# Kernel tuning notes

Measured on AMD Instinct MI355X. Metric: run time of the kernel, lower is better.

Reference implementation:

```python
import jax, jax.numpy as jnp
import numpy as np

B, S, D = 2, 2048, 2048
H, KVH, HD = 16, 4, 128
GROUPS = H // KVH
SCALE = HD ** -0.5


def rotate_half(x):
    half = x.shape[-1] // 2
    return jnp.concatenate((-x[..., half:], x[..., :half]), axis=-1)


def apply_rope(q, k, cos, sin):
    # q,k: [B,S,H,HD]; cos,sin: [S,HD//2] -> repeat_interleave(2) -> [S,HD]
    cos = jnp.repeat(cos, 2, axis=-1)[None, :, None, :]
    sin = jnp.repeat(sin, 2, axis=-1)[None, :, None, :]
    return q * cos + rotate_half(q) * sin, k * cos + rotate_half(k) * sin


def setup_inputs() -> dict:
    key = jax.random.key(0)
    ks = jax.random.split(key, 8)
    inp = {
        'x': jax.random.normal(ks[0], (B, S, D), dtype=jnp.float32),
        'cos': jnp.cos(jnp.arange(S, dtype=jnp.float32)[:, None] * (1.0 / (10000.0 ** (jnp.arange(HD // 2, dtype=jnp.float32) / (HD // 2))))[None, :].reshape(1, HD // 2)),
        'sin': None,
        'mask': jnp.tril(jnp.ones((S, S), dtype=bool))[None, None, :, :],
        'Wq': jax.random.normal(ks[1], (D, H * HD), dtype=jnp.float32) * (D ** -0.5),
        'Wk': jax.random.normal(ks[2], (D, KVH * HD), dtype=jnp.float32) * (D ** -0.5),
        'Wv': jax.random.normal(ks[3], (D, KVH * HD), dtype=jnp.float32) * (D ** -0.5),
        'Wo': jax.random.normal(ks[4], (H * HD, D), dtype=jnp.float32) * ((H * HD) ** -0.5),
    }
    inv_freq = 1.0 / (10000.0 ** (jnp.arange(0, HD // 2, dtype=jnp.float32) / (HD // 2)))
    freqs = jnp.arange(S, dtype=jnp.float32)[:, None] * inv_freq[None, :]  # [S, HD//2]
    inp['cos'] = jnp.cos(freqs)
    inp['sin'] = jnp.sin(freqs)
    return inp


def reference(x, cos, sin, mask, Wq, Wk, Wv, Wo):
    b, s, _ = x.shape
    q = (x @ Wq).reshape(b, s, H, HD)    # [B,S,H,HD]
    k = (x @ Wk).reshape(b, s, KVH, HD)  # [B,S,KVH,HD]
    v = (x @ Wv).reshape(b, s, KVH, HD)
    q, k = apply_rope(q, k, cos, sin)
    q = q.transpose(0, 2, 1, 3)  # [B,H,S,HD]
    k = k.transpose(0, 2, 1, 3)  # [B,KVH,S,HD]
    v = v.transpose(0, 2, 1, 3)
    k = jnp.repeat(k, GROUPS, axis=1)  # [B,H,S,HD]
    v = jnp.repeat(v, GROUPS, axis=1)
    scores = jnp.einsum('bhqd,bhkd->bhqk', q, k) * SCALE
    scores = jnp.where(mask, scores, -jnp.inf)
    attn = jax.nn.softmax(scores, axis=-1)
    out = jnp.einsum('bhqk,bhkd->bhqd', attn, v)
    out = out.transpose(0, 2, 1, 3).reshape(b, s, H * HD)
    return out @ Wo
```

## Files before the change

kernel.cpp:

```cpp
#include <hip/hip_runtime.h>
#include <hip/hip_bf16.h>
#include <cstdint>
#include <type_traits>

typedef __attribute__((ext_vector_type(8))) short short8;
typedef __attribute__((ext_vector_type(4))) float floatx4;

constexpr int S_LEN = 2048;
constexpr float ATTN_SCALE = 0.08838834764831845f;
constexpr float LOG2E = 1.4426950408889634f;
constexpr float CP = ATTN_SCALE * LOG2E;
constexpr float THRR = 5.0f / CP;

__device__ __forceinline__ void gl_lds16(const void* gp, void* lp) {
  __builtin_amdgcn_global_load_lds(
      (__attribute__((address_space(1))) void*)(uintptr_t)gp,
      (__attribute__((address_space(3))) void*)lp,
      16, 0, 0);
}

__device__ __forceinline__ void rope8(short8 x0, short8 x1, const float* ca,
                                      const float* sa, const float* cb,
                                      const float* sb, short8& y0, short8& y1) {
#pragma unroll
  for (int e = 0; e < 8; ++e) {
    union { short s; __hip_bfloat16 h; } u0, u1, w0, w1;
    u0.s = x0[e]; u1.s = x1[e];
    float f0 = __bfloat162float(u0.h), f1 = __bfloat162float(u1.h);
    int j = e >> 1;
    w0.h = __float2bfloat16(f0 * ca[j] - f1 * sa[j]);
    w1.h = __float2bfloat16(f1 * cb[j] + f0 * sb[j]);
    y0[e] = w0.s; y1[e] = w1.s;
  }
}

__device__ __forceinline__ void tr32(const float* __restrict__ src,
                                     __hip_bfloat16* __restrict__ dst,
                                     int blk, int nblk_x, int N, int tid,
                                     float (*tile)[33]) {
  int n0 = (blk % nblk_x) * 32, k0 = (blk / nblk_x) * 32;
  int tx = tid & 31, ty = tid >> 5;
#pragma unroll
  for (int i = ty; i < 32; i += 8)
    tile[i][tx] = src[(size_t)(k0 + i) * N + n0 + tx];
  __syncthreads();
#pragma unroll
  for (int i = ty; i < 32; i += 8)
    dst[(size_t)(n0 + i) * 2048 + k0 + tx] = __float2bfloat16(tile[tx][i]);
}

__global__ void prep_kernel(const float* __restrict__ x,
                            const float* __restrict__ Wq,
                            const float* __restrict__ Wk,
                            const float* __restrict__ Wv,
                            const float* __restrict__ Wo,
                            __hip_bfloat16* __restrict__ xb,
                            __hip_bfloat16* __restrict__ wqkvt,
                            __hip_bfloat16* __restrict__ wot) {
  __shared__ float tile[32][33];
  int bx = blockIdx.x, tid = threadIdx.x;
  if (bx < 8192) {
    int i = bx * 256 + tid;
    float4 f = reinterpret_cast<const float4*>(x)[i];
    union { unsigned long long u64; __hip_bfloat16 h[4]; } u;
    u.h[0] = __float2bfloat16(f.x);
    u.h[1] = __float2bfloat16(f.y);
    u.h[2] = __float2bfloat16(f.z);
    u.h[3] = __float2bfloat16(f.w);
    reinterpret_cast<unsigned long long*>(xb)[i] = u.u64;
  } else if (bx < 12288) {
    tr32(Wq, wqkvt, bx - 8192, 64, 2048, tid, tile);
  } else if (bx < 13312) {
    tr32(Wk, wqkvt + 2048 * 2048, bx - 12288, 16, 512, tid, tile);
  } else if (bx < 14336) {
    tr32(Wv, wqkvt + 2560 * 2048, bx - 13312, 16, 512, tid, tile);
  } else {
    tr32(Wo, wot, bx - 14336, 64, 2048, tid, tile);
  }
}

__device__ __forceinline__ void gemm256_core(
    const __hip_bfloat16* __restrict__ Ab,
    const __hip_bfloat16* __restrict__ Bb,
    const int K, __hip_bfloat16* lds, floatx4 (&acc)[8][4]) {
  const int tid = threadIdx.x;
  const int wave = tid >> 6, lane = tid & 63;
  const int quad = lane >> 4, l15 = lane & 15;
  const int wm = wave >> 2, wn = wave & 3;
  const int nt = K >> 6;
  const int u2 = wave * 2;

  auto stA = [&](int tt, int h) {
    __hip_bfloat16* dst = lds + (tt & 1) * 32768;
    const int k0 = tt << 6;
#pragma unroll
    for (int j = 0; j < 2; ++j) {
      const int kc = (u2 + j) >> 1, rb = (u2 + j) & 1;
      gl_lds16(Ab + (size_t)(h * 128 + rb * 64 + lane) * K + k0 + kc * 8,
               dst + (kc * 256 + h * 128 + rb * 64) * 8);
    }
  };
  auto stB = [&](int tt, int h) {
    __hip_bfloat16* dst = lds + (tt & 1) * 32768 + 16384;
    const int k0 = tt << 6;
#pragma unroll
    for (int j = 0; j < 2; ++j) {
      const int kc = (u2 + j) >> 1, rb = (u2 + j) & 1;
      gl_lds16(Bb + (size_t)(h * 128 + rb * 64 + lane) * K + k0 + kc * 8,
               dst + (kc * 256 + h * 128 + rb * 64) * 8);
    }
  };

  stA(0, 0); stA(0, 1); stB(0, 0); stB(0, 1);
  if (nt > 1) { stB(1, 0); stB(1, 1); }
  asm volatile("s_waitcnt vmcnt(4)" ::: "memory");
  __builtin_amdgcn_s_barrier();

  const int abase = (quad * 256 + wm * 128 + l15) * 8;
  const int bbase = (quad * 256 + wn * 64 + l15) * 8;

#pragma unroll 2
  for (int t = 0; t < nt; ++t) {
    const __hip_bfloat16* Al = lds + (t & 1) * 32768;
    const __hip_bfloat16* Bl = Al + 16384;
    short8 b[2][4];
#pragma unroll
    for (int q = 0; q < 4; ++q) {
      short8 a[2][2];
#pragma unroll
      for (int kk = 0; kk < 2; ++kk) {
        if (q == 0) {
#pragma unroll
          for (int ni = 0; ni < 4; ++ni)
            b[kk][ni] = *(const short8*)&Bl[kk * 8192 + bbase + ni * 128];
        }
#pragma unroll
        for (int mi = 0; mi < 2; ++mi)
          a[kk][mi] = *(const short8*)&Al[kk * 8192 + abase + (2 * q + mi) * 128];
      }
      if (q == 0)      { if (t + 1 < nt) stA(t + 1, 0); }
      else if (q == 1) { if (t + 1 < nt) stA(t + 1, 1); }
      else if (q == 2) { if (t + 2 < nt) stB(t + 2, 0); }
      else             { if (t + 2 < nt) stB(t + 2, 1); }
      __builtin_amdgcn_s_barrier();
      asm volatile("s_waitcnt lgkmcnt(0)" ::: "memory");
      __builtin_amdgcn_sched_barrier(0);
      __builtin_amdgcn_s_setprio(1);
#pragma unroll
      for (int kk = 0; kk < 2; ++kk)
#pragma unroll
        for (int mi = 0; mi < 2; ++mi)
#pragma unroll
          for (int ni = 0; ni < 4; ++ni)
            acc[2 * q + mi][ni] = __builtin_amdgcn_mfma_f32_16x16x32_bf16(
                a[kk][mi], b[kk][ni], acc[2 * q + mi][ni], 0, 0, 0);
      __builtin_amdgcn_s_setprio(0);
      if (q == 3) {
        if (t + 2 < nt) asm volatile("s_waitcnt vmcnt(4)" ::: "memory");
        else            asm volatile("s_waitcnt vmcnt(0)" ::: "memory");
      }
      __builtin_amdgcn_s_barrier();
    }
  }
  asm volatile("" ::: "memory");
}

__device__ __forceinline__ void gemm_256x128_core(
    const __hip_bfloat16* __restrict__ Ab,
    const __hip_bfloat16* __restrict__ Bb,
    const int K, __hip_bfloat16* lds, floatx4 (&acc)[4][4]) {
  const int tid = threadIdx.x;
  const int wave = tid >> 6, lane = tid & 63;
  const int quad = lane >> 4, l15 = lane & 15;
  const int wm = wave >> 1, wn = wave & 1;
  const int nt = K >> 6;

  auto stA = [&](int tt, int c) {
    __hip_bfloat16* dst = lds + (tt & 1) * 24576;
    const int k0 = tt << 6;
    const int i = c * 8 + wave;
    const int kc = i >> 2, rb = i & 3;
    gl_lds16(Ab + (size_t)(rb * 64 + lane) * K + k0 + kc * 8,
             dst + (kc * 256 + rb * 64) * 8);
  };
  auto stB = [&](int tt, int c) {
    __hip_bfloat16* dst = lds + (tt & 1) * 24576 + 16384;
    const int k0 = tt << 6;
    const int i = c * 8 + wave;
    const int kc = i >> 1, rb = i & 1;
    gl_lds16(Bb + (size_t)(rb * 64 + lane) * K + k0 + kc * 8,
             dst + (kc * 128 + rb * 64) * 8);
  };

  stA(0, 0); stA(0, 1); stA(0, 2); stA(0, 3);
  stB(0, 0); stB(0, 1);
  if (nt > 1) {
    stB(1, 0); stB(1, 1);
    asm volatile("s_waitcnt vmcnt(2)" ::: "memory");
  } else {
    asm volatile("s_waitcnt vmcnt(0)" ::: "memory");
  }
  __builtin_amdgcn_s_barrier();

  const int abase = (quad * 256 + wm * 64 + l15) * 8;
  const int bbase = (quad * 128 + wn * 64 + l15) * 8;

#pragma unroll 2
  for (int t = 0; t < nt; ++t) {
    const __hip_bfloat16* Al = lds + (t & 1) * 24576;
    const __hip_bfloat16* Bl = Al + 16384;
    short8 b[2][4], a[2][2];
#pragma unroll
    for (int kk = 0; kk < 2; ++kk) {
#pragma unroll
      for (int ni = 0; ni < 4; ++ni)
        b[kk][ni] = *(const short8*)&Bl[kk * 4096 + bbase + ni * 128];
#pragma unroll
      for (int mi = 0; mi < 2; ++mi)
        a[kk][mi] = *(const short8*)&Al[kk * 8192 + abase + mi * 128];
    }
    if (t + 1 < nt) { stA(t + 1, 0); stA(t + 1, 1); }
    __builtin_amdgcn_s_barrier();
    asm volatile("s_waitcnt lgkmcnt(0)" ::: "memory");
    __builtin_amdgcn_sched_barrier(0);
    __builtin_amdgcn_s_setprio(1);
#pragma unroll
    for (int kk = 0; kk < 2; ++kk)
#pragma unroll
      for (int mi = 0; mi < 2; ++mi)
#pragma unroll
        for (int ni = 0; ni < 4; ++ni)
          acc[mi][ni] = __builtin_amdgcn_mfma_f32_16x16x32_bf16(
              a[kk][mi], b[kk][ni], acc[mi][ni], 0, 0, 0);
    __builtin_amdgcn_s_setprio(0);
    __builtin_amdgcn_s_barrier();
#pragma unroll
    for (int kk = 0; kk < 2; ++kk)
#pragma unroll
      for (int mi = 0; mi < 2; ++mi)
        a[kk][mi] = *(const short8*)&Al[kk * 8192 + abase + (2 + mi) * 128];
    if (t + 1 < nt) { stA(t + 1, 2); stA(t + 1, 3); }
    if (t + 2 < nt) { stB(t + 2, 0); stB(t + 2, 1); }
    __builtin_amdgcn_s_barrier();
    asm volatile("s_waitcnt lgkmcnt(0)" ::: "memory");
    __builtin_amdgcn_sched_barrier(0);
    __builtin_amdgcn_s_setprio(1);
#pragma unroll
    for (int kk = 0; kk < 2; ++kk)
#pragma unroll
      for (int mi = 0; mi < 2; ++mi)
#pragma unroll
        for (int ni = 0; ni < 4; ++ni)
          acc[2 + mi][ni] = __builtin_amdgcn_mfma_f32_16x16x32_bf16(
              a[kk][mi], b[kk][ni], acc[2 + mi][ni], 0, 0, 0);
    __builtin_amdgcn_s_setprio(0);
    if (t + 2 < nt) asm volatile("s_waitcnt vmcnt(2)" ::: "memory");
    else            asm volatile("s_waitcnt vmcnt(0)" ::: "memory");
    __builtin_amdgcn_s_barrier();
  }
  asm volatile("" ::: "memory");
}

__global__ __launch_bounds__(512, 2) void qkv_gemm_kernel(
    const __hip_bfloat16* __restrict__ A,
    const __hip_bfloat16* __restrict__ Bt,
    __hip_bfloat16* __restrict__ qbuf,
    __hip_bfloat16* __restrict__ kbuf,
    __hip_bfloat16* __restrict__ vbuf,
    const float* __restrict__ cosb,
    const float* __restrict__ sinb) {
  constexpr int K = 2048;
  __shared__ __align__(16) __hip_bfloat16 lds[65536];
  const int tid = threadIdx.x;
  const int m0 = blockIdx.y * 256, n0 = blockIdx.x * 256;

  floatx4 acc[8][4] = {};
  gemm256_core(A + (size_t)m0 * K, Bt + (size_t)n0 * K, K, lds, acc);

  const int wave = tid >> 6, lane = tid & 63;
  const int quad = lane >> 4, l15 = lane & 15;
  const int wm = wave >> 2, wn = wave & 3;
  const bool isv = (n0 >= 2560);
  short* lds2 = (short*)lds;
#pragma unroll
  for (int mi = 0; mi < 8; ++mi)
#pragma unroll
    for (int ni = 0; ni < 4; ++ni)
#pragma unroll
      for (int r = 0; r < 4; ++r) {
        int row = wm * 128 + mi * 16 + quad * 4 + r;
        int col = wn * 64 + ni * 16 + l15;
        union { short s; __hip_bfloat16 h; } u;
        u.h = __float2bfloat16(acc[mi][ni][r]);
        if (isv) lds2[col * 256 + row] = u.s;
        else     lds2[row * 256 + col] = u.s;
      }
  __syncthreads();

  const int c16 = tid & 15, hh = c16 >> 3, c8 = c16 & 7;
  const int rid = tid >> 4, d0 = c8 * 8;
  if (n0 < 2048) {
#pragma unroll
    for (int j = 0; j < 8; ++j) {
      int rr = rid + 32 * j;
      int rowg = m0 + rr;
      int s = rowg & (S_LEN - 1);
      float ca[4], sa[4], cb[4], sb[4];
      *(float4*)ca = *(const float4*)&cosb[s * 64 + c8 * 4];
      *(float4*)sa = *(const float4*)&sinb[s * 64 + c8 * 4];
      *(float4*)cb = *(const float4*)&cosb[s * 64 + 32 + c8 * 4];
      *(float4*)sb = *(const float4*)&sinb[s * 64 + 32 + c8 * 4];
      short8 x0 = *(const short8*)&lds2[rr * 256 + hh * 128 + d0];
      short8 x1 = *(const short8*)&lds2[rr * 256 + hh * 128 + 64 + d0];
      short8 y0, y1;
      rope8(x0, x1, ca, sa, cb, sb, y0, y1);
      *(short8*)(qbuf + (size_t)rowg * 2048 + n0 + hh * 128 + d0) = y0;
      *(short8*)(qbuf + (size_t)rowg * 2048 + n0 + hh * 128 + 64 + d0) = y1;
    }
  } else if (!isv) {
    const int kvh = ((n0 - 2048) >> 7) + hh;
#pragma unroll
    for (int j = 0; j < 8; ++j) {
      int rr = rid + 32 * j;
      int rowg = m0 + rr;
      int s = rowg & (S_LEN - 1), bb = rowg >> 11;
      int kv = s & 63;
      size_t tb = ((size_t)(bb * 4 + kvh) * 32 + (s >> 6)) * 8192;
      float ca[4], sa[4], cb[4], sb[4];
      *(float4*)ca = *(const float4*)&cosb[s * 64 + c8 * 4];
      *(float4*)sa = *(const float4*)&sinb[s * 64 + c8 * 4];
      *(float4*)cb = *(const float4*)&cosb[s * 64 + 32 + c8 * 4];
      *(float4*)sb = *(const float4*)&sinb[s * 64 + 32 + c8 * 4];
      short8 x0 = *(const short8*)&lds2[rr * 256 + hh * 128 + d0];
      short8 x1 = *(const short8*)&lds2[rr * 256 + hh * 128 + 64 + d0];
      short8 y0, y1;
      rope8(x0, x1, ca, sa, cb, sb, y0, y1);
      *(short8*)(kbuf + tb + (size_t)c8 * 512 + kv * 8) = y0;
      *(short8*)(kbuf + tb + (size_t)(8 + c8) * 512 + kv * 8) = y1;
    }
  } else {
    const int kvh = ((n0 - 2560) >> 7) + hh;
    const int bb = m0 >> 11;
    const int kt0 = (m0 & (S_LEN - 1)) >> 6;
    const int kv0 = c8 * 8;
#pragma unroll
    for (int j = 0; j < 4; ++j) {
      int d = rid + 32 * j;
      int cxor = (d & 7) << 3;
#pragma unroll
      for (int half = 0; half < 4; ++half) {
        short8 vv = *(const short8*)&lds2[(hh * 128 + d) * 256 + half * 64 + kv0];
        size_t tb = ((size_t)(bb * 4 + kvh) * 32 + kt0 + half) * 8192;
        *(short8*)(vbuf + tb + d * 64 + (kv0 ^ cxor)) = vv;
      }
    }
  }
}

__global__ __launch_bounds__(512, 2) void gemm_bt_f32_kernel(
    const __hip_bfloat16* __restrict__ A,
    const __hip_bfloat16* __restrict__ Bt,
    float* __restrict__ C, int N, int K) {
  __shared__ __align__(16) __hip_bfloat16 lds[49152];
  const int tid = threadIdx.x;
  const int m0 = blockIdx.y * 256, n0 = blockIdx.x * 128;

  floatx4 acc[4][4] = {};
  gemm_256x128_core(A + (size_t)m0 * K, Bt + (size_t)n0 * K, K, lds, acc);

  const int wave = tid >> 6, lane = tid & 63;
  const int quad = lane >> 4, l15 = lane & 15;
  const int wm = wave >> 1, wn = wave & 1;
#pragma unroll
  for (int mi = 0; mi < 4; ++mi)
#pragma unroll
    for (int ni = 0; ni < 4; ++ni)
#pragma unroll
      for (int r = 0; r < 4; ++r) {
        int row = m0 + wm * 64 + mi * 16 + quad * 4 + r;
        int col = n0 + wn * 64 + ni * 16 + l15;
        C[(size_t)row * N + col] = acc[mi][ni][r];
      }
}

__global__ __launch_bounds__(256, 2) void attn_kernel(
    const __hip_bfloat16* __restrict__ qbuf,
    const __hip_bfloat16* __restrict__ kbuf,
    const __hip_bfloat16* __restrict__ vbuf,
    __hip_bfloat16* __restrict__ aout) {
  const int qt = (blockIdx.y & 16) ? blockIdx.x : (15 - blockIdx.x);
  const int bh = blockIdx.y;
  const int b = bh >> 4, h = bh & 15;
  const int kvh = h >> 2;

  __shared__ __align__(16) __hip_bfloat16 Kbuf[2][8192];
  __shared__ __align__(16) __hip_bfloat16 Vbuf[2][8192];

  const int tid = threadIdx.x;
  const int wave = tid >> 6, lane = tid & 63;
  const int quad = lane >> 4, l15 = lane & 15;

  short8 qfrag[2][4];
#pragma unroll
  for (int rs = 0; rs < 2; ++rs)
#pragma unroll
    for (int kc = 0; kc < 4; ++kc)
      qfrag[rs][kc] = *(const short8*)(qbuf +
          (size_t)(b * S_LEN + qt * 128 + rs * 64 + wave * 16 + l15) * 2048 +
          h * 128 + kc * 32 + quad * 8);

  const __hip_bfloat16* ktiles = kbuf + (size_t)(b * 4 + kvh) * 32 * 8192;
  const __hip_bfloat16* vtiles = vbuf + (size_t)(b * 4 + kvh) * 32 * 8192;
  const int nt = 2 * qt + 2;

#pragma unroll
  for (int j = 0; j < 4; ++j) {
    int c = tid + 256 * j;
    gl_lds16(ktiles + c * 8, &Kbuf[0][c * 8]);
    gl_lds16(vtiles + c * 8, &Vbuf[0][c * 8]);
  }

  float m_s[2] = {-1e30f, -1e30f};
  float l_s[2] = {0.f, 0.f};
  floatx4 o[2][8] = {};

  for (int kt = 0; kt < nt; ++kt) {
    const int cur = kt & 1;
    __syncthreads();

    if (kt + 1 < nt) {
      const __hip_bfloat16* kb = ktiles + (size_t)(kt + 1) * 8192;
      const __hip_bfloat16* vb = vtiles + (size_t)(kt + 1) * 8192;
#pragma unroll
      for (int j = 0; j < 4; ++j) {
        int c = tid + 256 * j;
        gl_lds16(kb + c * 8, &Kbuf[1 - cur][c * 8]);
        gl_lds16(vb + c * 8, &Vbuf[1 - cur][c * 8]);
      }
    }

    floatx4 sc[2][4] = {};
#pragma unroll
    for (int ni = 0; ni < 4; ++ni)
#pragma unroll
      for (int kc = 0; kc < 4; ++kc) {
        short8 bf = *(const short8*)&Kbuf[cur][((kc * 4 + quad) * 64 + ni * 16 + l15) * 8];
        sc[0][ni] = __builtin_amdgcn_mfma_f32_16x16x32_bf16(bf, qfrag[0][kc], sc[0][ni], 0, 0, 0);
        sc[1][ni] = __builtin_amdgcn_mfma_f32_16x16x32_bf16(bf, qfrag[1][kc], sc[1][ni], 0, 0, 0);
      }

    short8 pa[2][2];
#pragma unroll
    for (int rs = 0; rs < 2; ++rs) {
      const int qt64 = 2 * qt + rs;
      if (kt >= qt64) {
        const int qg = qt * 128 + rs * 64 + wave * 16 + l15;
#pragma unroll
        for (int ni = 0; ni < 4; ++ni) {
          int kvb = kt * 64 + ni * 16 + quad * 4;
#pragma unroll
          for (int r = 0; r < 4; ++r)
            if (kvb + r > qg) sc[rs][ni][r] = -1e30f;
        }
      }

      float v = sc[rs][0][0];
#pragma unroll
      for (int ni = 0; ni < 4; ++ni)
#pragma unroll
        for (int r = 0; r < 4; ++r) v = fmaxf(v, sc[rs][ni][r]);
      v = fmaxf(v, __shfl_xor(v, 16));
      v = fmaxf(v, __shfl_xor(v, 32));

      float mold = m_s[rs];
      if (__any(v > mold + THRR)) {
        float mnew = fmaxf(mold, v);
        float alpha = exp2f((mold - mnew) * CP);
        m_s[rs] = mnew;
        l_s[rs] *= alpha;
        float ar[4];
#pragma unroll
        for (int r = 0; r < 4; ++r)
          ar[r] = __shfl(alpha, (lane & 48) + quad * 4 + r);
#pragma unroll
        for (int nc = 0; nc < 8; ++nc)
#pragma unroll
          for (int r = 0; r < 4; ++r) o[rs][nc][r] *= ar[r];
      }

      float mc = m_s[rs] * CP;
      unsigned pk[4][2];
      float lsum = 0.f;
#pragma unroll
      for (int ni = 0; ni < 4; ++ni)
#pragma unroll
        for (int pr = 0; pr < 2; ++pr) {
          float p0 = exp2f(sc[rs][ni][2 * pr] * CP - mc);
          float p1 = exp2f(sc[rs][ni][2 * pr + 1] * CP - mc);
          lsum += p0 + p1;
          union { unsigned u; ushort us[2]; } uu;
          union { __hip_bfloat16 h; ushort us; } b0, b1;
          b0.h = __float2bfloat16(p0); b1.h = __float2bfloat16(p1);
          uu.us[0] = b0.us; uu.us[1] = b1.us;
          pk[ni][pr] = uu.u;
        }
      lsum += __shfl_xor(lsum, 16);
      lsum += __shfl_xor(lsum, 32);
      l_s[rs] += lsum;

#pragma unroll
      for (int kk2 = 0; kk2 < 2; ++kk2) {
        union { unsigned w[4]; short8 s; } pw_;
#pragma unroll
        for (int j = 0; j < 4; ++j) {
          int src = ((((quad & 1) * 2) + (j >> 1)) << 4) | l15;
          unsigned lo = (unsigned)__shfl((int)pk[2 * kk2][j & 1], src);
          unsigned hi = (unsigned)__shfl((int)pk[2 * kk2 + 1][j & 1], src);
          pw_.w[j] = (quad >> 1) ? hi : lo;
        }
        pa[rs][kk2] = pw_.s;
      }
    }

#pragma unroll
    for (int kk2 = 0; kk2 < 2; ++kk2) {
#pragma unroll
      for (int nc = 0; nc < 8; ++nc) {
        int d = nc * 16 + l15;
        int swcol = (kk2 * 32 + quad * 8) ^ ((d & 7) << 3);
        short8 vv = *(const short8*)&Vbuf[cur][d * 64 + swcol];
        o[0][nc] = __builtin_amdgcn_mfma_f32_16x16x32_bf16(pa[0][kk2], vv, o[0][nc], 0, 0, 0);
        o[1][nc] = __builtin_amdgcn_mfma_f32_16x16x32_bf16(pa[1][kk2], vv, o[1][nc], 0, 0, 0);
      }
    }
  }

#pragma unroll
  for (int rs = 0; rs < 2; ++rs) {
    float inv[4];
#pragma unroll
    for (int r = 0; r < 4; ++r) {
      float lr = __shfl(l_s[rs], (lane & 48) + quad * 4 + r);
      inv[r] = 1.0f / lr;
    }
    const size_t orow0 = (size_t)(b * S_LEN + qt * 128 + rs * 64 + wave * 16 + quad * 4);
#pragma unroll
    for (int nc = 0; nc < 8; ++nc)
#pragma unroll
      for (int r = 0; r < 4; ++r)
        aout[(orow0 + r) * 2048 + h * 128 + nc * 16 + l15] =
            __float2bfloat16(o[rs][nc][r] * inv[r]);
  }
}

extern "C" void kernel_launch(void* const* d_in, const int* in_sizes, int n_in,
                              void* d_out, int out_size, void* d_ws, size_t ws_size,
                              hipStream_t stream) {
  const float* x    = (const float*)d_in[0];
  const float* cosb = (const float*)d_in[1];
  const float* sinb = (const float*)d_in[2];
  const float* Wq = (const float*)d_in[4];
  const float* Wk = (const float*)d_in[5];
  const float* Wv = (const float*)d_in[6];
  const float* Wo = (const float*)d_in[7];
  float* out = (float*)d_out;

  char* ws = (char*)d_ws;
  __hip_bfloat16* xb    = (__hip_bfloat16*)(ws);
  __hip_bfloat16* wqkvt = (__hip_bfloat16*)(ws + (16u << 20));
  __hip_bfloat16* wot   = (__hip_bfloat16*)(ws + (28u << 20));
  __hip_bfloat16* qbuf  = (__hip_bfloat16*)(ws + (36u << 20));
  __hip_bfloat16* kbuf  = (__hip_bfloat16*)(ws + (52u << 20));
  __hip_bfloat16* vbuf  = (__hip_bfloat16*)(ws + (56u << 20));
  __hip_bfloat16* aout  = (__hip_bfloat16*)(ws + (60u << 20));

  prep_kernel<<<18432, 256, 0, stream>>>(x, Wq, Wk, Wv, Wo, xb, wqkvt, wot);
  qkv_gemm_kernel<<<dim3(12, 16), 512, 0, stream>>>(xb, wqkvt, qbuf, kbuf, vbuf, cosb, sinb);
  attn_kernel<<<dim3(16, 32), 256, 0, stream>>>(qbuf, kbuf, vbuf, aout);
  gemm_bt_f32_kernel<<<dim3(16, 16), 512, 0, stream>>>(aout, wot, out, 2048, 2048);
}
```

Measured before the change: 366.7 us.

## Software-pipeline QK of next tile with softmax/PV, split K/V prefetch barriers

Restructures the attention inner loop so the QK^T MFMAs for tile i+1 are issued before softmax and PV of tile i, letting matrix work overlap the softmax math. K and V loads are issued separately with explicit vmcnt waits and raw barriers, so each buffer is refilled as soon as it is free. It also skips MFMAs for the first 64-row half once that half is fully masked, and raises wave priority around the PV MFMAs. This adds register pressure from the extra score accumulators and relies on hand-counted vmcnt values being correct.

```diff
diff --git a/kernel.cpp b/kernel.cpp
--- a/kernel.cpp
+++ b/kernel.cpp
@@ -413,51 +413,65 @@
   const __hip_bfloat16* vtiles = vbuf + (size_t)(b * 4 + kvh) * 32 * 8192;
   const int nt = 2 * qt + 2;
 
-#pragma unroll
-  for (int j = 0; j < 4; ++j) {
-    int c = tid + 256 * j;
-    gl_lds16(ktiles + c * 8, &Kbuf[0][c * 8]);
-    gl_lds16(vtiles + c * 8, &Vbuf[0][c * 8]);
-  }
+  auto SK = [&](int t) {
+#pragma unroll
+    for (int j = 0; j < 4; ++j) {
+      int c = tid + 256 * j;
+      gl_lds16(ktiles + (size_t)t * 8192 + c * 8, &Kbuf[t & 1][c * 8]);
+    }
+  };
+  auto SV = [&](int t) {
+#pragma unroll
+    for (int j = 0; j < 4; ++j) {
+      int c = tid + 256 * j;
+      gl_lds16(vtiles + (size_t)t * 8192 + c * 8, &Vbuf[t & 1][c * 8]);
+    }
+  };
+
+  auto QK = [&](const __hip_bfloat16* Kc, floatx4 (&s)[2][4], bool q0) {
+#pragma unroll
+    for (int ni = 0; ni < 4; ++ni)
+#pragma unroll
+      for (int kc = 0; kc < 4; ++kc) {
+        short8 bf = *(const short8*)&Kc[((kc * 4 + quad) * 64 + ni * 16 + l15) * 8];
+        if (q0)
+          s[0][ni] = __builtin_amdgcn_mfma_f32_16x16x32_bf16(bf, qfrag[0][kc], s[0][ni], 0, 0, 0);
+        s[1][ni] = __builtin_amdgcn_mfma_f32_16x16x32_bf16(bf, qfrag[1][kc], s[1][ni], 0, 0, 0);
+      }
+  };
+
+  SK(0); SV(0);
+  SK(1); SV(1);
+  asm volatile("s_waitcnt vmcnt(12)" ::: "memory");
+  __builtin_amdgcn_s_barrier();
 
   float m_s[2] = {-1e30f, -1e30f};
   float l_s[2] = {0.f, 0.f};
   floatx4 o[2][8] = {};
 
-  for (int kt = 0; kt < nt; ++kt) {
-    const int cur = kt & 1;
-    __syncthreads();
-
-    if (kt + 1 < nt) {
-      const __hip_bfloat16* kb = ktiles + (size_t)(kt + 1) * 8192;
-      const __hip_bfloat16* vb = vtiles + (size_t)(kt + 1) * 8192;
-#pragma unroll
-      for (int j = 0; j < 4; ++j) {
-        int c = tid + 256 * j;
-        gl_lds16(kb + c * 8, &Kbuf[1 - cur][c * 8]);
-        gl_lds16(vb + c * 8, &Vbuf[1 - cur][c * 8]);
-      }
-    }
-
-    floatx4 sc[2][4] = {};
-#pragma unroll
-    for (int ni = 0; ni < 4; ++ni)
-#pragma unroll
-      for (int kc = 0; kc < 4; ++kc) {
-        short8 bf = *(const short8*)&Kbuf[cur][((kc * 4 + quad) * 64 + ni * 16 + l15) * 8];
-        sc[0][ni] = __builtin_amdgcn_mfma_f32_16x16x32_bf16(bf, qfrag[0][kc], sc[0][ni], 0, 0, 0);
-        sc[1][ni] = __builtin_amdgcn_mfma_f32_16x16x32_bf16(bf, qfrag[1][kc], sc[1][ni], 0, 0, 0);
-      }
-
+  floatx4 sc[2][4] = {};
+  QK(Kbuf[0], sc, true);
+
+  for (int i = 0; i < nt; ++i) {
+    if (i + 1 < nt) asm volatile("s_waitcnt vmcnt(4)" ::: "memory");
+    else            asm volatile("s_waitcnt vmcnt(0)" ::: "memory");
+    __builtin_amdgcn_s_barrier();
+    if (i + 2 < nt) SK(i + 2);
+
+    floatx4 sc2[2][4] = {};
+    if (i + 1 < nt) QK(Kbuf[(i + 1) & 1], sc2, (i + 1) <= 2 * qt);
+
+    const bool do0 = (i <= 2 * qt);
     short8 pa[2][2];
 #pragma unroll
     for (int rs = 0; rs < 2; ++rs) {
+      if (rs == 0 && !do0) continue;
       const int qt64 = 2 * qt + rs;
-      if (kt >= qt64) {
+      if (i >= qt64) {
         const int qg = qt * 128 + rs * 64 + wave * 16 + l15;
 #pragma unroll
         for (int ni = 0; ni < 4; ++ni) {
-          int kvb = kt * 64 + ni * 16 + quad * 4;
+          int kvb = i * 64 + ni * 16 + quad * 4;
 #pragma unroll
           for (int r = 0; r < 4; ++r)
             if (kvb + r > qg) sc[rs][ni][r] = -1e30f;
@@ -522,17 +536,29 @@
       }
     }
 
+    __builtin_amdgcn_s_setprio(1);
 #pragma unroll
     for (int kk2 = 0; kk2 < 2; ++kk2) {
 #pragma unroll
       for (int nc = 0; nc < 8; ++nc) {
         int d = nc * 16 + l15;
         int swcol = (kk2 * 32 + quad * 8) ^ ((d & 7) << 3);
-        short8 vv = *(const short8*)&Vbuf[cur][d * 64 + swcol];
-        o[0][nc] = __builtin_amdgcn_mfma_f32_16x16x32_bf16(pa[0][kk2], vv, o[0][nc], 0, 0, 0);
+        short8 vv = *(const short8*)&Vbuf[i & 1][d * 64 + swcol];
+        if (do0)
+          o[0][nc] = __builtin_amdgcn_mfma_f32_16x16x32_bf16(pa[0][kk2], vv, o[0][nc], 0, 0, 0);
         o[1][nc] = __builtin_amdgcn_mfma_f32_16x16x32_bf16(pa[1][kk2], vv, o[1][nc], 0, 0, 0);
       }
     }
+    __builtin_amdgcn_s_setprio(0);
+
+    asm volatile("" ::: "memory");
+    __builtin_amdgcn_s_barrier();
+    if (i + 2 < nt) SV(i + 2);
+
+#pragma unroll
+    for (int rs = 0; rs < 2; ++rs)
+#pragma unroll
+      for (int ni = 0; ni < 4; ++ni) sc[rs][ni] = sc2[rs][ni];
   }
 
 #pragma unroll
```

Measured after the change: 383.0 us. +4.5%, slower.

## Halve attention query tile, read V fragments directly from global memory

Applied to the files above, without the earlier changes.

The attention kernel now processes 64 query rows per block instead of 128, doubling the grid and raising the occupancy hint to 4 blocks per CU. V is no longer staged through LDS. The QKV epilogue writes V in an MFMA-fragment-ready layout so each lane loads its B operand straight from global memory, with raised wave priority around the PV MFMAs. This trades LDS usage and sync cost for more parallelism, but reloads K/V tiles twice as often across blocks and puts global-load latency directly in the PV loop.

```diff
diff --git a/kernel.cpp b/kernel.cpp
--- a/kernel.cpp
+++ b/kernel.cpp
@@ -346,12 +346,12 @@
 #pragma unroll
     for (int j = 0; j < 4; ++j) {
       int d = rid + 32 * j;
-      int cxor = (d & 7) << 3;
 #pragma unroll
       for (int half = 0; half < 4; ++half) {
         short8 vv = *(const short8*)&lds2[(hh * 128 + d) * 256 + half * 64 + kv0];
         size_t tb = ((size_t)(bb * 4 + kvh) * 32 + kt0 + half) * 8192;
-        *(short8*)(vbuf + tb + d * 64 + (kv0 ^ cxor)) = vv;
+        *(short8*)(vbuf + tb + ((c8 >> 2) * 8 + (d >> 4)) * 512
+                        + ((c8 & 3) * 16 + (d & 15)) * 8) = vv;
       }
     }
   }
@@ -383,174 +383,153 @@
       }
 }
 
-__global__ __launch_bounds__(256, 2) void attn_kernel(
+__global__ __launch_bounds__(256, 4) void attn_kernel(
     const __hip_bfloat16* __restrict__ qbuf,
     const __hip_bfloat16* __restrict__ kbuf,
     const __hip_bfloat16* __restrict__ vbuf,
     __hip_bfloat16* __restrict__ aout) {
-  const int qt = (blockIdx.y & 16) ? blockIdx.x : (15 - blockIdx.x);
+  const int qt = (blockIdx.y & 16) ? blockIdx.x : (31 - blockIdx.x);
   const int bh = blockIdx.y;
   const int b = bh >> 4, h = bh & 15;
   const int kvh = h >> 2;
 
   __shared__ __align__(16) __hip_bfloat16 Kbuf[2][8192];
-  __shared__ __align__(16) __hip_bfloat16 Vbuf[2][8192];
 
   const int tid = threadIdx.x;
   const int wave = tid >> 6, lane = tid & 63;
   const int quad = lane >> 4, l15 = lane & 15;
 
-  short8 qfrag[2][4];
-#pragma unroll
-  for (int rs = 0; rs < 2; ++rs)
-#pragma unroll
-    for (int kc = 0; kc < 4; ++kc)
-      qfrag[rs][kc] = *(const short8*)(qbuf +
-          (size_t)(b * S_LEN + qt * 128 + rs * 64 + wave * 16 + l15) * 2048 +
-          h * 128 + kc * 32 + quad * 8);
+  short8 qfrag[4];
+#pragma unroll
+  for (int kc = 0; kc < 4; ++kc)
+    qfrag[kc] = *(const short8*)(qbuf +
+        (size_t)(b * S_LEN + qt * 64 + wave * 16 + l15) * 2048 +
+        h * 128 + kc * 32 + quad * 8);
 
   const __hip_bfloat16* ktiles = kbuf + (size_t)(b * 4 + kvh) * 32 * 8192;
   const __hip_bfloat16* vtiles = vbuf + (size_t)(b * 4 + kvh) * 32 * 8192;
-  const int nt = 2 * qt + 2;
-
-#pragma unroll
-  for (int j = 0; j < 4; ++j) {
-    int c = tid + 256 * j;
-    gl_lds16(ktiles + c * 8, &Kbuf[0][c * 8]);
-    gl_lds16(vtiles + c * 8, &Vbuf[0][c * 8]);
-  }
-
-  float m_s[2] = {-1e30f, -1e30f};
-  float l_s[2] = {0.f, 0.f};
-  floatx4 o[2][8] = {};
-
-  for (int kt = 0; kt < nt; ++kt) {
-    const int cur = kt & 1;
+  const int nt = qt + 1;
+
+  auto SK = [&](int t) {
+#pragma unroll
+    for (int j = 0; j < 4; ++j) {
+      int c = tid + 256 * j;
+      gl_lds16(ktiles + (size_t)t * 8192 + c * 8, &Kbuf[t & 1][c * 8]);
+    }
+  };
+
+  SK(0);
+
+  float m_s = -1e30f, l_s = 0.f;
+  floatx4 o[8] = {};
+
+  for (int i = 0; i < nt; ++i) {
     __syncthreads();
-
-    if (kt + 1 < nt) {
-      const __hip_bfloat16* kb = ktiles + (size_t)(kt + 1) * 8192;
-      const __hip_bfloat16* vb = vtiles + (size_t)(kt + 1) * 8192;
+    if (i + 1 < nt) SK(i + 1);
+
+    floatx4 sc[4] = {};
+#pragma unroll
+    for (int ni = 0; ni < 4; ++ni)
+#pragma unroll
+      for (int kc = 0; kc < 4; ++kc) {
+        short8 bf = *(const short8*)&Kbuf[i & 1][((kc * 4 + quad) * 64 + ni * 16 + l15) * 8];
+        sc[ni] = __builtin_amdgcn_mfma_f32_16x16x32_bf16(bf, qfrag[kc], sc[ni], 0, 0, 0);
+      }
+
+    if (i == qt) {
+      const int qg = qt * 64 + wave * 16 + l15;
+#pragma unroll
+      for (int ni = 0; ni < 4; ++ni) {
+        int kvb = i * 64 + ni * 16 + quad * 4;
+#pragma unroll
+        for (int r = 0; r < 4; ++r)
+          if (kvb + r > qg) sc[ni][r] = -1e30f;
+      }
+    }
+
+    float v = sc[0][0];
+#pragma unroll
+    for (int ni = 0; ni < 4; ++ni)
+#pragma unroll
+      for (int r = 0; r < 4; ++r) v = fmaxf(v, sc[ni][r]);
+    v = fmaxf(v, __shfl_xor(v, 16));
+    v = fmaxf(v, __shfl_xor(v, 32));
+
+    float mold = m_s;
+    if (__any(v > mold + THRR)) {
+      float mnew = fmaxf(mold, v);
+      float alpha = exp2f((mold - mnew) * CP);
+      m_s = mnew;
+      l_s *= alpha;
+      float ar[4];
+#pragma unroll
+      for (int r = 0; r < 4; ++r)
+        ar[r] = __shfl(alpha, (lane & 48) + quad * 4 + r);
+#pragma unroll
+      for (int nc = 0; nc < 8; ++nc)
+#pragma unroll
+        for (int r = 0; r < 4; ++r) o[nc][r] *= ar[r];
+    }
+
+    float mc = m_s * CP;
+    unsigned pk[4][2];
+    float lsum = 0.f;
+#pragma unroll
+    for (int ni = 0; ni < 4; ++ni)
+#pragma unroll
+      for (int pr = 0; pr < 2; ++pr) {
+        float p0 = exp2f(sc[ni][2 * pr] * CP - mc);
+        float p1 = exp2f(sc[ni][2 * pr + 1] * CP - mc);
+        lsum += p0 + p1;
+        union { unsigned u; ushort us[2]; } uu;
+        union { __hip_bfloat16 h; ushort us; } b0, b1;
+        b0.h = __float2bfloat16(p0); b1.h = __float2bfloat16(p1);
+        uu.us[0] = b0.us; uu.us[1] = b1.us;
+        pk[ni][pr] = uu.u;
+      }
+    lsum += __shfl_xor(lsum, 16);
+    lsum += __shfl_xor(lsum, 32);
+    l_s += lsum;
+
+    short8 pa[2];
+#pragma unroll
+    for (int kk2 = 0; kk2 < 2; ++kk2) {
+      union { unsigned w[4]; short8 s; } pw_;
 #pragma unroll
       for (int j = 0; j < 4; ++j) {
-        int c = tid + 256 * j;
-        gl_lds16(kb + c * 8, &Kbuf[1 - cur][c * 8]);
-        gl_lds16(vb + c * 8, &Vbuf[1 - cur][c * 8]);
-      }
-    }
-
-    floatx4 sc[2][4] = {};
-#pragma unroll
-    for (int ni = 0; ni < 4; ++ni)
-#pragma unroll
-      for (int kc = 0; kc < 4; ++kc) {
-        short8 bf = *(const short8*)&Kbuf[cur][((kc * 4 + quad) * 64 + ni * 16 + l15) * 8];
-        sc[0][ni] = __builtin_amdgcn_mfma_f32_16x16x32_bf16(bf, qfrag[0][kc], sc[0][ni], 0, 0, 0);
-        sc[1][ni] = __builtin_amdgcn_mfma_f32_16x16x32_bf16(bf, qfrag[1][kc], sc[1][ni], 0, 0, 0);
-      }
-
-    short8 pa[2][2];
-#pragma unroll
-    for (int rs = 0; rs < 2; ++rs) {
-      const int qt64 = 2 * qt + rs;
-      if (kt >= qt64) {
-        const int qg = qt * 128 + rs * 64 + wave * 16 + l15;
-#pragma unroll
-        for (int ni = 0; ni < 4; ++ni) {
-          int kvb = kt * 64 + ni * 16 + quad * 4;
-#pragma unroll
-          for (int r = 0; r < 4; ++r)
-            if (kvb + r > qg) sc[rs][ni][r] = -1e30f;
-        }
-      }
-
-      float v = sc[rs][0][0];
-#pragma unroll
-      for (int ni = 0; ni < 4; ++ni)
-#pragma unroll
-        for (int r = 0; r < 4; ++r) v = fmaxf(v, sc[rs][ni][r]);
-      v = fmaxf(v, __shfl_xor(v, 16));
-      v = fmaxf(v, __shfl_xor(v, 32));
-
-      float mold = m_s[rs];
-      if (__any(v > mold + THRR)) {
-        float mnew = fmaxf(mold, v);
-        float alpha = exp2f((mold - mnew) * CP);
-        m_s[rs] = mnew;
-        l_s[rs] *= alpha;
-        float ar[4];
-#pragma unroll
-        for (int r = 0; r < 4; ++r)
-          ar[r] = __shfl(alpha, (lane & 48) + quad * 4 + r);
-#pragma unroll
-        for (int nc = 0; nc < 8; ++nc)
-#pragma unroll
-          for (int r = 0; r < 4; ++r) o[rs][nc][r] *= ar[r];
-      }
-
-      float mc = m_s[rs] * CP;
-      unsigned pk[4][2];
-      float lsum = 0.f;
-#pragma unroll
-      for (int ni = 0; ni < 4; ++ni)
-#pragma unroll
-        for (int pr = 0; pr < 2; ++pr) {
-          float p0 = exp2f(sc[rs][ni][2 * pr] * CP - mc);
-          float p1 = exp2f(sc[rs][ni][2 * pr + 1] * CP - mc);
-          lsum += p0 + p1;
-          union { unsigned u; ushort us[2]; } uu;
-          union { __hip_bfloat16 h; ushort us; } b0, b1;
-          b0.h = __float2bfloat16(p0); b1.h = __float2bfloat16(p1);
-          uu.us[0] = b0.us; uu.us[1] = b1.us;
-          pk[ni][pr] = uu.u;
-        }
-      lsum += __shfl_xor(lsum, 16);
-      lsum += __shfl_xor(lsum, 32);
-      l_s[rs] += lsum;
-
-#pragma unroll
-      for (int kk2 = 0; kk2 < 2; ++kk2) {
-        union { unsigned w[4]; short8 s; } pw_;
-#pragma unroll
-        for (int j = 0; j < 4; ++j) {
-          int src = ((((quad & 1) * 2) + (j >> 1)) << 4) | l15;
-          unsigned lo = (unsigned)__shfl((int)pk[2 * kk2][j & 1], src);
-          unsigned hi = (unsigned)__shfl((int)pk[2 * kk2 + 1][j & 1], src);
-          pw_.w[j] = (quad >> 1) ? hi : lo;
-        }
-        pa[rs][kk2] = pw_.s;
-      }
-    }
-
-#pragma unroll
-    for (int kk2 = 0; kk2 < 2; ++kk2) {
+        int src = ((((quad & 1) * 2) + (j >> 1)) << 4) | l15;
+        unsigned lo = (unsigned)__shfl((int)pk[2 * kk2][j & 1], src);
+        unsigned hi = (unsigned)__shfl((int)pk[2 * kk2 + 1][j & 1], src);
+        pw_.w[j] = (quad >> 1) ? hi : lo;
+      }
+      pa[kk2] = pw_.s;
+    }
+
+    const __hip_bfloat16* vt = vtiles + (size_t)i * 8192;
+    __builtin_amdgcn_s_setprio(1);
+#pragma unroll
+    for (int kk2 = 0; kk2 < 2; ++kk2)
 #pragma unroll
       for (int nc = 0; nc < 8; ++nc) {
-        int d = nc * 16 + l15;
-        int swcol = (kk2 * 32 + quad * 8) ^ ((d & 7) << 3);
-        short8 vv = *(const short8*)&Vbuf[cur][d * 64 + swcol];
-        o[0][nc] = __builtin_amdgcn_mfma_f32_16x16x32_bf16(pa[0][kk2], vv, o[0][nc], 0, 0, 0);
-        o[1][nc] = __builtin_amdgcn_mfma_f32_16x16x32_bf16(pa[1][kk2], vv, o[1][nc], 0, 0, 0);
-      }
-    }
-  }
-
-#pragma unroll
-  for (int rs = 0; rs < 2; ++rs) {
-    float inv[4];
-#pragma unroll
-    for (int r = 0; r < 4; ++r) {
-      float lr = __shfl(l_s[rs], (lane & 48) + quad * 4 + r);
-      inv[r] = 1.0f / lr;
-    }
-    const size_t orow0 = (size_t)(b * S_LEN + qt * 128 + rs * 64 + wave * 16 + quad * 4);
-#pragma unroll
-    for (int nc = 0; nc < 8; ++nc)
-#pragma unroll
-      for (int r = 0; r < 4; ++r)
-        aout[(orow0 + r) * 2048 + h * 128 + nc * 16 + l15] =
-            __float2bfloat16(o[rs][nc][r] * inv[r]);
-  }
+        short8 vv = *(const short8*)&vt[((kk2 * 8 + nc) * 64 + quad * 16 + l15) * 8];
+        o[nc] = __builtin_amdgcn_mfma_f32_16x16x32_bf16(pa[kk2], vv, o[nc], 0, 0, 0);
+      }
+    __builtin_amdgcn_s_setprio(0);
+  }
+
+  float inv[4];
+#pragma unroll
+  for (int r = 0; r < 4; ++r) {
+    float lr = __shfl(l_s, (lane & 48) + quad * 4 + r);
+    inv[r] = 1.0f / lr;
+  }
+  const size_t orow0 = (size_t)(b * S_LEN + qt * 64 + wave * 16 + quad * 4);
+#pragma unroll
+  for (int nc = 0; nc < 8; ++nc)
+#pragma unroll
+    for (int r = 0; r < 4; ++r)
+      aout[(orow0 + r) * 2048 + h * 128 + nc * 16 + l15] =
+          __float2bfloat16(o[nc][r] * inv[r]);
 }
 
 extern "C" void kernel_launch(void* const* d_in, const int* in_sizes, int n_in,
@@ -576,6 +555,6 @@
 
   prep_kernel<<<18432, 256, 0, stream>>>(x, Wq, Wk, Wv, Wo, xb, wqkvt, wot);
   qkv_gemm_kernel<<<dim3(12, 16), 512, 0, stream>>>(xb, wqkvt, qbuf, kbuf, vbuf, cosb, sinb);
-  attn_kernel<<<dim3(16, 32), 256, 0, stream>>>(qbuf, kbuf, vbuf, aout);
+  attn_kernel<<<dim3(32, 32), 256, 0, stream>>>(qbuf, kbuf, vbuf, aout);
   gemm_bt_f32_kernel<<<dim3(16, 16), 512, 0, stream>>>(aout, wot, out, 2048, 2048);
 }
```

Result: slower. 385.6 us (+5.2%).

## Stream V fragments from global in MFMA layout, widen KV tile to 128

Applied to the files above, without the earlier changes.

The V projection epilogue now writes V in a fragment-ready layout, so the attention kernel can load V operands straight from global or L2 into registers instead of staging them through LDS. The KV tile per iteration doubles to 128 keys, which halves the number of loop iterations and barriers and lets K use the whole freed LDS. V loads are software-pipelined across the four PV MFMA groups and wrapped in raised wave priority. This raises register pressure and exposes V loads to global latency in exchange for less LDS traffic and fewer syncs.

```diff
diff --git a/kernel.cpp b/kernel.cpp
--- a/kernel.cpp
+++ b/kernel.cpp
@@ -346,12 +346,12 @@
 #pragma unroll
     for (int j = 0; j < 4; ++j) {
       int d = rid + 32 * j;
-      int cxor = (d & 7) << 3;
 #pragma unroll
       for (int half = 0; half < 4; ++half) {
         short8 vv = *(const short8*)&lds2[(hh * 128 + d) * 256 + half * 64 + kv0];
         size_t tb = ((size_t)(bb * 4 + kvh) * 32 + kt0 + half) * 8192;
-        *(short8*)(vbuf + tb + d * 64 + (kv0 ^ cxor)) = vv;
+        *(short8*)(vbuf + tb + ((c8 >> 2) * 8 + (d >> 4)) * 512
+                        + ((c8 & 3) * 16 + (d & 15)) * 8) = vv;
       }
     }
   }
@@ -393,8 +393,7 @@
   const int b = bh >> 4, h = bh & 15;
   const int kvh = h >> 2;
 
-  __shared__ __align__(16) __hip_bfloat16 Kbuf[2][8192];
-  __shared__ __align__(16) __hip_bfloat16 Vbuf[2][8192];
+  __shared__ __align__(16) __hip_bfloat16 Kbuf[2][16384];
 
   const int tid = threadIdx.x;
   const int wave = tid >> 6, lane = tid & 63;
@@ -411,53 +410,53 @@
 
   const __hip_bfloat16* ktiles = kbuf + (size_t)(b * 4 + kvh) * 32 * 8192;
   const __hip_bfloat16* vtiles = vbuf + (size_t)(b * 4 + kvh) * 32 * 8192;
-  const int nt = 2 * qt + 2;
-
-#pragma unroll
-  for (int j = 0; j < 4; ++j) {
-    int c = tid + 256 * j;
-    gl_lds16(ktiles + c * 8, &Kbuf[0][c * 8]);
-    gl_lds16(vtiles + c * 8, &Vbuf[0][c * 8]);
-  }
+  const int nt = qt + 1;
+
+  auto SK = [&](int t) {
+#pragma unroll
+    for (int j = 0; j < 8; ++j) {
+      int c = tid + 256 * j;
+      gl_lds16(ktiles + (size_t)(2 * t) * 8192 + c * 8, &Kbuf[t & 1][c * 8]);
+    }
+  };
+
+  SK(0);
 
   float m_s[2] = {-1e30f, -1e30f};
   float l_s[2] = {0.f, 0.f};
   floatx4 o[2][8] = {};
 
-  for (int kt = 0; kt < nt; ++kt) {
-    const int cur = kt & 1;
+  for (int i = 0; i < nt; ++i) {
     __syncthreads();
-
-    if (kt + 1 < nt) {
-      const __hip_bfloat16* kb = ktiles + (size_t)(kt + 1) * 8192;
-      const __hip_bfloat16* vb = vtiles + (size_t)(kt + 1) * 8192;
-#pragma unroll
-      for (int j = 0; j < 4; ++j) {
-        int c = tid + 256 * j;
-        gl_lds16(kb + c * 8, &Kbuf[1 - cur][c * 8]);
-        gl_lds16(vb + c * 8, &Vbuf[1 - cur][c * 8]);
-      }
-    }
-
-    floatx4 sc[2][4] = {};
-#pragma unroll
-    for (int ni = 0; ni < 4; ++ni)
+    if (i + 1 < nt) SK(i + 1);
+
+    floatx4 sc[2][8] = {};
+#pragma unroll
+    for (int ni = 0; ni < 8; ++ni)
 #pragma unroll
       for (int kc = 0; kc < 4; ++kc) {
-        short8 bf = *(const short8*)&Kbuf[cur][((kc * 4 + quad) * 64 + ni * 16 + l15) * 8];
+        short8 bf = *(const short8*)&Kbuf[i & 1][
+            (ni >> 2) * 8192 + ((kc * 4 + quad) * 64 + (ni & 3) * 16 + l15) * 8];
         sc[0][ni] = __builtin_amdgcn_mfma_f32_16x16x32_bf16(bf, qfrag[0][kc], sc[0][ni], 0, 0, 0);
         sc[1][ni] = __builtin_amdgcn_mfma_f32_16x16x32_bf16(bf, qfrag[1][kc], sc[1][ni], 0, 0, 0);
       }
 
-    short8 pa[2][2];
+    const __hip_bfloat16* vt = vtiles + (size_t)(2 * i) * 8192;
+    const int vl = quad * 16 + l15;
+    short8 va[8], vb[8];
+#pragma unroll
+    for (int nc = 0; nc < 8; ++nc)
+      va[nc] = *(const short8*)&vt[(nc * 64 + vl) * 8];
+
+    const bool diag = (i == qt);
+    short8 pa[2][4];
 #pragma unroll
     for (int rs = 0; rs < 2; ++rs) {
-      const int qt64 = 2 * qt + rs;
-      if (kt >= qt64) {
+      if (diag) {
         const int qg = qt * 128 + rs * 64 + wave * 16 + l15;
 #pragma unroll
-        for (int ni = 0; ni < 4; ++ni) {
-          int kvb = kt * 64 + ni * 16 + quad * 4;
+        for (int ni = 0; ni < 8; ++ni) {
+          int kvb = i * 128 + ni * 16 + quad * 4;
 #pragma unroll
           for (int r = 0; r < 4; ++r)
             if (kvb + r > qg) sc[rs][ni][r] = -1e30f;
@@ -466,7 +465,7 @@
 
       float v = sc[rs][0][0];
 #pragma unroll
-      for (int ni = 0; ni < 4; ++ni)
+      for (int ni = 0; ni < 8; ++ni)
 #pragma unroll
         for (int r = 0; r < 4; ++r) v = fmaxf(v, sc[rs][ni][r]);
       v = fmaxf(v, __shfl_xor(v, 16));
@@ -489,10 +488,10 @@
       }
 
       float mc = m_s[rs] * CP;
-      unsigned pk[4][2];
+      unsigned pk[8][2];
       float lsum = 0.f;
 #pragma unroll
-      for (int ni = 0; ni < 4; ++ni)
+      for (int ni = 0; ni < 8; ++ni)
 #pragma unroll
         for (int pr = 0; pr < 2; ++pr) {
           float p0 = exp2f(sc[rs][ni][2 * pr] * CP - mc);
@@ -509,7 +508,7 @@
       l_s[rs] += lsum;
 
 #pragma unroll
-      for (int kk2 = 0; kk2 < 2; ++kk2) {
+      for (int kk2 = 0; kk2 < 4; ++kk2) {
         union { unsigned w[4]; short8 s; } pw_;
 #pragma unroll
         for (int j = 0; j < 4; ++j) {
@@ -522,17 +521,37 @@
       }
     }
 
-#pragma unroll
-    for (int kk2 = 0; kk2 < 2; ++kk2) {
-#pragma unroll
-      for (int nc = 0; nc < 8; ++nc) {
-        int d = nc * 16 + l15;
-        int swcol = (kk2 * 32 + quad * 8) ^ ((d & 7) << 3);
-        short8 vv = *(const short8*)&Vbuf[cur][d * 64 + swcol];
-        o[0][nc] = __builtin_amdgcn_mfma_f32_16x16x32_bf16(pa[0][kk2], vv, o[0][nc], 0, 0, 0);
-        o[1][nc] = __builtin_amdgcn_mfma_f32_16x16x32_bf16(pa[1][kk2], vv, o[1][nc], 0, 0, 0);
-      }
-    }
+    __builtin_amdgcn_s_setprio(1);
+#pragma unroll
+    for (int nc = 0; nc < 8; ++nc)
+      vb[nc] = *(const short8*)&vt[((8 + nc) * 64 + vl) * 8];
+#pragma unroll
+    for (int nc = 0; nc < 8; ++nc) {
+      o[0][nc] = __builtin_amdgcn_mfma_f32_16x16x32_bf16(pa[0][0], va[nc], o[0][nc], 0, 0, 0);
+      o[1][nc] = __builtin_amdgcn_mfma_f32_16x16x32_bf16(pa[1][0], va[nc], o[1][nc], 0, 0, 0);
+    }
+#pragma unroll
+    for (int nc = 0; nc < 8; ++nc)
+      va[nc] = *(const short8*)&vt[8192 + (nc * 64 + vl) * 8];
+#pragma unroll
+    for (int nc = 0; nc < 8; ++nc) {
+      o[0][nc] = __builtin_amdgcn_mfma_f32_16x16x32_bf16(pa[0][1], vb[nc], o[0][nc], 0, 0, 0);
+      o[1][nc] = __builtin_amdgcn_mfma_f32_16x16x32_bf16(pa[1][1], vb[nc], o[1][nc], 0, 0, 0);
+    }
+#pragma unroll
+    for (int nc = 0; nc < 8; ++nc)
+      vb[nc] = *(const short8*)&vt[8192 + ((8 + nc) * 64 + vl) * 8];
+#pragma unroll
+    for (int nc = 0; nc < 8; ++nc) {
+      o[0][nc] = __builtin_amdgcn_mfma_f32_16x16x32_bf16(pa[0][2], va[nc], o[0][nc], 0, 0, 0);
+      o[1][nc] = __builtin_amdgcn_mfma_f32_16x16x32_bf16(pa[1][2], va[nc], o[1][nc], 0, 0, 0);
+    }
+#pragma unroll
+    for (int nc = 0; nc < 8; ++nc) {
+      o[0][nc] = __builtin_amdgcn_mfma_f32_16x16x32_bf16(pa[0][3], vb[nc], o[0][nc], 0, 0, 0);
+      o[1][nc] = __builtin_amdgcn_mfma_f32_16x16x32_bf16(pa[1][3], vb[nc], o[1][nc], 0, 0, 0);
+    }
+    __builtin_amdgcn_s_setprio(0);
   }
 
 #pragma unroll
```

Result: slower. 398.7 us (+8.7%).
